# Kernel optimization log

Measured on AMD Instinct MI355X. Metric: run time of the kernel, lower is better.

The kernel has to match this reference:

```python
import jax, jax.numpy as jnp
import numpy as np

NUM_OP = 2048      # num_op_unary + (num_feature-1)*num_op_binary + 1 = 7 + 255*8 + 1
NUM_ACTION = 1024  # num_feature * max_order = 256 * 4
NUM_BATCH = 32


def setup_inputs() -> dict:
    key = jax.random.key(0)
    k = jax.random.split(key, 6)
    s = 1.0 / np.sqrt(NUM_OP)  # torch LSTM init scale
    W_ih = jax.random.uniform(k[0], (4 * NUM_OP, NUM_OP), jnp.float32, -s, s)
    W_hh = jax.random.uniform(k[1], (4 * NUM_OP, NUM_OP), jnp.float32, -s, s)
    b_ih = jax.random.uniform(k[2], (4 * NUM_OP,), jnp.float32, -s, s)
    b_hh = jax.random.uniform(k[3], (4 * NUM_OP,), jnp.float32, -s, s)
    rewards = jax.random.normal(k[4], (NUM_BATCH,), jnp.float32)
    action = jax.random.randint(k[5], (NUM_BATCH, NUM_ACTION), 0, NUM_OP, dtype=jnp.int64)
    return {"W_ih": W_ih, "W_hh": W_hh, "b_ih": b_ih, "b_hh": b_hh,
            "rewards": rewards, "action": action}


def reference(W_ih, W_hh, b_ih, b_hh, rewards, action):
    # The torch forward only sets tmp_input at step 0, so the SAME constant
    # input0 = ones/num_op is fed to the LSTM at every step. Its contribution
    # to the gates is therefore a constant vector, precomputed once.
    x0 = jnp.full((NUM_OP,), 1.0 / NUM_OP, dtype=W_ih.dtype)
    x_gates = x0 @ W_ih.T + b_ih + b_hh  # [4*num_op]

    def cell(carry, _):
        h, c = carry
        g = x_gates + h @ W_hh.T                       # [4*num_op]
        i, f, gg, o = jnp.split(g, 4)                  # torch gate order i,f,g,o
        i = jax.nn.sigmoid(i)
        f = jax.nn.sigmoid(f)
        gg = jnp.tanh(gg)
        o = jax.nn.sigmoid(o)
        c = f * c + i * gg
        h = o * jnp.tanh(c)
        return (h, c), h

    init = (jnp.zeros((NUM_OP,), W_ih.dtype), jnp.zeros((NUM_OP,), W_ih.dtype))
    _, outputs = jax.lax.scan(cell, init, None, length=NUM_ACTION)  # [A, num_op]

    logp = jax.nn.log_softmax(outputs, axis=-1)        # [A, num_op]
    probs = jnp.exp(logp)
    entropy_sum = -jnp.sum(probs * logp)               # scalar, identical per batch

    # gather log-prob of each taken action: [B, A]
    gathered = logp[jnp.arange(NUM_ACTION)[None, :], action]
    reinforce = -jnp.sum(gathered * rewards[:, None])
    loss = (reinforce + NUM_BATCH * entropy_sum) / NUM_BATCH
    return loss
```

## Files before the change

kernel.cpp:

```cpp
#include <hip/hip_runtime.h>

#define NOP   2048
#define NACT  1024
#define NB    32
#define NBLK  256
#define NTHR  320

typedef _Float16 f16;
typedef _Float16 h2t __attribute__((ext_vector_type(2)));
typedef unsigned long long u64t;
typedef unsigned int u32t;


template <int CTRL>
__device__ __forceinline__ float dpp_add(float x) {
  union { float f; int i; } a, r;
  a.f = x;
  r.i = __builtin_amdgcn_update_dpp(0, a.i, CTRL, 0xF, 0xF, true);
  return x + r.f;
}

__device__ __forceinline__ float wave_sum63(float x) {
  x = dpp_add<0x111>(x);
  x = dpp_add<0x112>(x);
  x = dpp_add<0x114>(x);
  x = dpp_add<0x118>(x);
  x = dpp_add<0x142>(x);
  x = dpp_add<0x143>(x);
  return x;
}

__device__ __forceinline__ float dot8(float4 wv, float4 hv, float acc) {
  union U { float f; h2t v; };
  U w0{wv.x}, w1{wv.y}, w2{wv.z}, w3{wv.w};
  U h0{hv.x}, h1{hv.y}, h2{hv.z}, h3{hv.w};
#if __has_builtin(__builtin_amdgcn_fdot2)
  acc = __builtin_amdgcn_fdot2(w0.v, h0.v, acc, false);
  acc = __builtin_amdgcn_fdot2(w1.v, h1.v, acc, false);
  acc = __builtin_amdgcn_fdot2(w2.v, h2.v, acc, false);
  acc = __builtin_amdgcn_fdot2(w3.v, h3.v, acc, false);
#else
  acc += (float)w0.v.x * (float)h0.v.x + (float)w0.v.y * (float)h0.v.y;
  acc += (float)w1.v.x * (float)h1.v.x + (float)w1.v.y * (float)h1.v.y;
  acc += (float)w2.v.x * (float)h2.v.x + (float)w2.v.y * (float)h2.v.y;
  acc += (float)w3.v.x * (float)h3.v.x + (float)w3.v.y * (float)h3.v.y;
#endif
  return acc;
}

__device__ __forceinline__ float sigmoid_f(float x) {
  return 1.0f / (1.0f + __expf(-x));
}
__device__ __forceinline__ float tanh_f(float x) {
  float ax = fabsf(x);
  float e = __expf(-2.0f * ax);
  float r = (1.0f - e) / (1.0f + e);
  return copysignf(r, x);
}

__device__ __forceinline__ void lds_bar(int* ctr, int target, int ln) {
  __threadfence_block();
  if (ln == 0)
    __hip_atomic_fetch_add(ctr, 1, __ATOMIC_RELAXED, __HIP_MEMORY_SCOPE_WORKGROUP);
  while (__hip_atomic_load(ctr, __ATOMIC_RELAXED, __HIP_MEMORY_SCOPE_WORKGROUP) <
         target) {}
  __threadfence_block();
}

extern "C" __global__ __launch_bounds__(256) void prep_pack(
    const float* __restrict__ Whh, f16* __restrict__ Wp) {
  int tid = blockIdx.x * 256 + threadIdx.x;
  int l = tid & 63;
  int c = (tid >> 6) & 3;
  int r = (tid >> 8) & 7;
  int w = (tid >> 11) & 3;
  int b = tid >> 13;
  int gate = r >> 1, jj = r & 1;
  int grow = gate * NOP + b * 8 + w * 2 + jj;
  int k = l * 32 + c * 8;
  const float4* src = (const float4*)(Whh + (size_t)grow * NOP + k);
  float4 a = src[0], b2 = src[1];
  union { f16 h[8]; float4 v; } o;
  o.h[0] = (f16)a.x;  o.h[1] = (f16)a.y;  o.h[2] = (f16)a.z;  o.h[3] = (f16)a.w;
  o.h[4] = (f16)b2.x; o.h[5] = (f16)b2.y; o.h[6] = (f16)b2.z; o.h[7] = (f16)b2.w;
  ((float4*)Wp)[tid] = o.v;
}

extern "C" __global__ void __launch_bounds__(NTHR) lstm_main(
    const float* __restrict__ Wih, const float* __restrict__ bih,
    const float* __restrict__ bhh, const f16* __restrict__ Wp,
    float* __restrict__ outputs, u64t* __restrict__ glob,
    u64t* __restrict__ sumf) {
  extern __shared__ char smem[];
  f16*  w_lds = (f16*)smem;
  u32t* h2    = (u32t*)(smem + 131072);
  int*  barA  = (int*)(smem + 131072 + 9184);

  const int b  = blockIdx.x;
  const int w  = threadIdx.x >> 6;
  const int ln = threadIdx.x & 63;

  if (threadIdx.x == 0) *barA = 0;

  if (w < 4) {
    const float4* src = (const float4*)(Wp + (size_t)b * 65536) + w * 2048;
    float4* dst = (float4*)w_lds + w * 2048;
    for (int i = ln; i < 2048; i += 64) dst[i] = src[i];
  }
  __syncthreads();

  if (w == 4) {
    if (b >= 8) return;
    for (int tau = 1; tau < NACT; ++tau) {
      const int par = (tau - 1) & 1;
      const u64t* src = glob + (size_t)par * 1024 + b * 128 + ln * 2;
      const u32t want = (u32t)tau;
      for (;;) {
        u64t x0 = __hip_atomic_load(src + 0, __ATOMIC_RELAXED, __HIP_MEMORY_SCOPE_AGENT);
        u64t x1 = __hip_atomic_load(src + 1, __ATOMIC_RELAXED, __HIP_MEMORY_SCOPE_AGENT);
        bool good = (((u32t)x0 - want) <= 4u) & (((u32t)x1 - want) <= 4u);
        if (__all(good)) break;
      }
      if (ln == 0)
        __hip_atomic_store(&sumf[par * 8 + b], (u64t)want,
                           __ATOMIC_RELEASE, __HIP_MEMORY_SCOPE_AGENT);
    }
    return;
  }

  float xg[8];
#pragma unroll
  for (int r = 0; r < 8; ++r) {
    int gate = r >> 1, jj = r & 1;
    int grow = gate * NOP + b * 8 + w * 2 + jj;
    const float4* src = (const float4*)(Wih + (size_t)grow * NOP) + ln * 8;
    float s = 0.f;
#pragma unroll
    for (int q = 0; q < 8; ++q) {
      float4 v = src[q];
      s += v.x + v.y + v.z + v.w;
    }
    s = wave_sum63(s);
    xg[r] = s * (1.0f / NOP) + bih[grow] + bhh[grow];
  }

  float c0 = 0.f, c1 = 0.f;

  for (int t = 0; t < NACT; ++t) {
    float S[8];
    if (t > 0) {
      const int par = (t - 1) & 1;
      const u32t want = (u32t)t;
      {
        int spins = 0;
        for (;;) {
          bool ok = true;
          if (ln < 8) {
            u64t fv = __hip_atomic_load(&sumf[par * 8 + ln], __ATOMIC_RELAXED,
                                        __HIP_MEMORY_SCOPE_AGENT);
            ok = (((u32t)fv - want) <= 4u);
          }
          if (__all(ok)) break;
          if (++spins > 2048) break;
        }
      }
      const u64t* base = glob + (size_t)par * 1024 + w * 256 + ln * 4;
      u64t x0, x1, x2, x3;
      for (;;) {
        x0 = __hip_atomic_load(base + 0, __ATOMIC_RELAXED, __HIP_MEMORY_SCOPE_AGENT);
        x1 = __hip_atomic_load(base + 1, __ATOMIC_RELAXED, __HIP_MEMORY_SCOPE_AGENT);
        x2 = __hip_atomic_load(base + 2, __ATOMIC_RELAXED, __HIP_MEMORY_SCOPE_AGENT);
        x3 = __hip_atomic_load(base + 3, __ATOMIC_RELAXED, __HIP_MEMORY_SCOPE_AGENT);
        bool good = ((u32t)x0 == want) & ((u32t)x1 == want) &
                    ((u32t)x2 == want) & ((u32t)x3 == want);
        if (__all(good)) break;
      }
      uint4* hp4 = (uint4*)(h2 + par * 1148);
      {
        uint4 pay;
        pay.x = (u32t)(x0 >> 32); pay.y = (u32t)(x1 >> 32);
        pay.z = (u32t)(x2 >> 32); pay.w = (u32t)(x3 >> 32);
        int Q = 64 * w + ln;
        hp4[Q + (Q >> 3)] = pay;
      }
      lds_bar(barA, 4 * t, ln);

      float4 hreg[4];
#pragma unroll
      for (int c = 0; c < 4; ++c) {
        int Q = 4 * ln + c;
        hreg[c] = *((const float4*)hp4 + (Q + (Q >> 3)));
      }
#pragma unroll
      for (int r = 0; r < 8; ++r) {
        float acc = 0.f;
#pragma unroll
        for (int c = 0; c < 4; ++c) {
          float4 wv = *((const float4*)(
              w_lds + (((((w * 8 + r) * 4) + c) * 64 + ln) * 8)));
          acc = dot8(wv, hreg[c], acc);
        }
        S[r] = wave_sum63(acc) + xg[r];
      }
    } else {
#pragma unroll
      for (int r = 0; r < 8; ++r) S[r] = xg[r];
    }

    float i0 = sigmoid_f(S[0]), i1 = sigmoid_f(S[1]);
    float f0 = sigmoid_f(S[2]), f1 = sigmoid_f(S[3]);
    float g0 = tanh_f(S[4]),    g1 = tanh_f(S[5]);
    float o0 = sigmoid_f(S[6]), o1 = sigmoid_f(S[7]);
    c0 = f0 * c0 + i0 * g0;
    c1 = f1 * c1 + i1 * g1;
    float h0 = o0 * tanh_f(c0);
    float h1 = o1 * tanh_f(c1);

    if (ln == 63) {
      if (t < NACT - 1) {
        union { f16 q[2]; u32t u; } pk;
        pk.q[0] = (f16)h0; pk.q[1] = (f16)h1;
        u64t val = ((u64t)pk.u << 32) | (u64t)(u32t)(t + 1);
        __hip_atomic_store(glob + (size_t)(t & 1) * 1024 + 4 * b + w, val,
                           __ATOMIC_RELAXED, __HIP_MEMORY_SCOPE_AGENT);
      }
      float2 hv; hv.x = h0; hv.y = h1;
      *((float2*)(outputs + (size_t)t * NOP + b * 8 + w * 2)) = hv;
    }
  }
}

extern "C" __global__ __launch_bounds__(256) void phase2(
    const float* __restrict__ outputs, const float* __restrict__ rewards,
    const int* __restrict__ action, float* __restrict__ accum) {
  __shared__ float sm[4], s1s[4], s2s[4];
  __shared__ float bc[2];
  const int t = blockIdx.x, tid = threadIdx.x, w = tid >> 6, ln = tid & 63;
  const float* row = outputs + (size_t)t * NOP;
  const float4* r4 = (const float4*)row;
  float4 a = r4[tid], b4 = r4[tid + 256];

  float m = fmaxf(fmaxf(fmaxf(a.x, a.y), fmaxf(a.z, a.w)),
                  fmaxf(fmaxf(b4.x, b4.y), fmaxf(b4.z, b4.w)));
#pragma unroll
  for (int off = 32; off >= 1; off >>= 1) m = fmaxf(m, __shfl_xor(m, off));
  if (ln == 0) sm[w] = m;
  __syncthreads();
  if (tid == 0) bc[0] = fmaxf(fmaxf(sm[0], sm[1]), fmaxf(sm[2], sm[3]));
  __syncthreads();
  const float M = bc[0];

  float s1 = 0.f, s2 = 0.f;
  {
    float xs[8] = {a.x, a.y, a.z, a.w, b4.x, b4.y, b4.z, b4.w};
#pragma unroll
    for (int u = 0; u < 8; ++u) {
      float d = xs[u] - M;
      float p = __expf(d);
      s1 += p;
      s2 += d * p;
    }
  }
#pragma unroll
  for (int off = 32; off >= 1; off >>= 1) {
    s1 += __shfl_xor(s1, off);
    s2 += __shfl_xor(s2, off);
  }
  if (ln == 0) { s1s[w] = s1; s2s[w] = s2; }
  __syncthreads();
  if (tid == 0) {
    float S1 = s1s[0] + s1s[1] + s1s[2] + s1s[3];
    float S2 = s2s[0] + s2s[1] + s2s[2] + s2s[3];
    float lse = M + logf(S1);
    atomicAdd(&accum[1], logf(S1) - S2 / S1);
    bc[1] = lse;
  }
  __syncthreads();
  if (tid < 32) {
    int ai = action[tid * NACT + t] & (NOP - 1);
    float val = row[ai] - bc[1];
    float rr = rewards[tid] * val;
#pragma unroll
    for (int off = 16; off >= 1; off >>= 1) rr += __shfl_xor(rr, off);
    if (tid == 0) atomicAdd(&accum[0], rr);
  }
}

extern "C" __global__ void finalize(const float* __restrict__ accum,
                                    float* __restrict__ out) {
  out[0] = accum[1] - accum[0] * (1.0f / NB);
}

extern "C" void kernel_launch(void* const* d_in, const int* in_sizes, int n_in,
                              void* d_out, int out_size, void* d_ws, size_t ws_size,
                              hipStream_t stream) {
  const float* W_ih    = (const float*)d_in[0];
  const float* W_hh    = (const float*)d_in[1];
  const float* b_ih    = (const float*)d_in[2];
  const float* b_hh    = (const float*)d_in[3];
  const float* rewards = (const float*)d_in[4];
  const int*   action  = (const int*)d_in[5];

  char* ws = (char*)d_ws;
  u64t*  glob    = (u64t*)ws;
  u64t*  sumf    = (u64t*)(ws + 16 * 1024);
  float* accum   = (float*)(ws + 20 * 1024);
  float* outputs = (float*)(ws + 8u * 1024 * 1024);
  f16*   Wp      = (f16*)(ws + 16u * 1024 * 1024);

  hipMemsetAsync(accum, 0, 256, stream);

  hipLaunchKernelGGL(prep_pack, dim3(8192), dim3(256), 0, stream, W_hh, Wp);

  const unsigned smem = 131072 + 9184 + 16;
  hipFuncSetAttribute((const void*)lstm_main,
                      hipFuncAttributeMaxDynamicSharedMemorySize, (int)smem);
  void* args[] = {(void*)&W_ih, (void*)&b_ih, (void*)&b_hh, (void*)&Wp,
                  (void*)&outputs, (void*)&glob, (void*)&sumf};
  hipLaunchCooperativeKernel((void*)lstm_main, dim3(NBLK), dim3(NTHR), args,
                             smem, stream);

  hipLaunchKernelGGL(phase2, dim3(NACT), dim3(256), 0, stream,
                     outputs, rewards, action, accum);
  hipLaunchKernelGGL(finalize, dim3(1), dim3(1), 0, stream, accum, (float*)d_out);
}
```

Before: 4.656 ms.

## Replace eight-aggregator summary flags with single aggregator broadcasting per-block flags

The grid-wide step barrier changes shape. Eight aggregator waves each used to check part of the hidden-state slots and publish a summary flag, which every block polled across 8 entries. Now a single aggregator wave on block 0 checks all 1024 slots and writes a dedicated flag for each block, each on its own 128-byte line, so every block polls just one line with one lane. This is meant to cut polling traffic and contention on shared flag lines, at the cost of a longer serial check in one wave and 256 flag stores per step.

```diff
diff --git a/kernel.cpp b/kernel.cpp
--- a/kernel.cpp
+++ b/kernel.cpp
@@ -90,7 +90,7 @@
     const float* __restrict__ Wih, const float* __restrict__ bih,
     const float* __restrict__ bhh, const f16* __restrict__ Wp,
     float* __restrict__ outputs, u64t* __restrict__ glob,
-    u64t* __restrict__ sumf) {
+    u64t* __restrict__ bflag) {
   extern __shared__ char smem[];
   f16*  w_lds = (f16*)smem;
   u32t* h2    = (u32t*)(smem + 131072);
@@ -110,20 +110,26 @@
   __syncthreads();
 
   if (w == 4) {
-    if (b >= 8) return;
+    if (b != 0) return;
     for (int tau = 1; tau < NACT; ++tau) {
       const int par = (tau - 1) & 1;
-      const u64t* src = glob + (size_t)par * 1024 + b * 128 + ln * 2;
+      const u64t* src = glob + (size_t)par * 1024 + ln * 16;
       const u32t want = (u32t)tau;
       for (;;) {
-        u64t x0 = __hip_atomic_load(src + 0, __ATOMIC_RELAXED, __HIP_MEMORY_SCOPE_AGENT);
-        u64t x1 = __hip_atomic_load(src + 1, __ATOMIC_RELAXED, __HIP_MEMORY_SCOPE_AGENT);
-        bool good = (((u32t)x0 - want) <= 4u) & (((u32t)x1 - want) <= 4u);
+        bool good = true;
+        u64t x[16];
+#pragma unroll
+        for (int i = 0; i < 16; ++i)
+          x[i] = __hip_atomic_load(src + i, __ATOMIC_RELAXED,
+                                   __HIP_MEMORY_SCOPE_AGENT);
+#pragma unroll
+        for (int i = 0; i < 16; ++i) good &= (((u32t)x[i] - want) <= 4u);
         if (__all(good)) break;
       }
-      if (ln == 0)
-        __hip_atomic_store(&sumf[par * 8 + b], (u64t)want,
-                           __ATOMIC_RELEASE, __HIP_MEMORY_SCOPE_AGENT);
+#pragma unroll
+      for (int q = 0; q < 4; ++q)
+        __hip_atomic_store(bflag + (size_t)(ln * 4 + q) * 16, (u64t)want,
+                           __ATOMIC_RELAXED, __HIP_MEMORY_SCOPE_AGENT);
     }
     return;
   }
@@ -145,6 +151,7 @@
   }
 
   float c0 = 0.f, c1 = 0.f;
+  const u64t* myflag = bflag + (size_t)b * 16;
 
   for (int t = 0; t < NACT; ++t) {
     float S[8];
@@ -154,14 +161,10 @@
       {
         int spins = 0;
         for (;;) {
-          bool ok = true;
-          if (ln < 8) {
-            u64t fv = __hip_atomic_load(&sumf[par * 8 + ln], __ATOMIC_RELAXED,
-                                        __HIP_MEMORY_SCOPE_AGENT);
-            ok = (((u32t)fv - want) <= 4u);
-          }
-          if (__all(ok)) break;
-          if (++spins > 2048) break;
+          u64t fv = __hip_atomic_load(myflag, __ATOMIC_RELAXED,
+                                      __HIP_MEMORY_SCOPE_AGENT);
+          if (((u32t)fv - want) <= 4u) break;
+          if (++spins > 8192) break;
         }
       }
       const u64t* base = glob + (size_t)par * 1024 + w * 256 + ln * 4;
@@ -303,12 +306,12 @@
 
   char* ws = (char*)d_ws;
   u64t*  glob    = (u64t*)ws;
-  u64t*  sumf    = (u64t*)(ws + 16 * 1024);
-  float* accum   = (float*)(ws + 20 * 1024);
+  u64t*  bflag   = (u64t*)(ws + 16 * 1024);
+  float* accum   = (float*)(ws + 48 * 1024);
   float* outputs = (float*)(ws + 8u * 1024 * 1024);
   f16*   Wp      = (f16*)(ws + 16u * 1024 * 1024);
 
-  hipMemsetAsync(accum, 0, 256, stream);
+  hipMemsetAsync(ws + 16 * 1024, 0, 32 * 1024 + 256, stream);
 
   hipLaunchKernelGGL(prep_pack, dim3(8192), dim3(256), 0, stream, W_hh, Wp);
 
@@ -316,7 +319,7 @@
   hipFuncSetAttribute((const void*)lstm_main,
                       hipFuncAttributeMaxDynamicSharedMemorySize, (int)smem);
   void* args[] = {(void*)&W_ih, (void*)&b_ih, (void*)&b_hh, (void*)&Wp,
-                  (void*)&outputs, (void*)&glob, (void*)&sumf};
+                  (void*)&outputs, (void*)&glob, (void*)&bflag};
   hipLaunchCooperativeKernel((void*)lstm_main, dim3(NBLK), dim3(NTHR), args,
                              smem, stream);
 
```

Measured after the change: 4.664 ms. About the same (+0.2%).
